# Kernel tuning notes

Hardware: AMD Instinct MI355X
Metric: run time of the kernel (lower is better)

Reference implementation:

```python
import jax, jax.numpy as jnp
import numpy as np

HEAD_SIZE = 128
N_EMBD = 128
B, T = 16, 2048


def setup_inputs() -> dict:
    key = jax.random.key(0)
    ks = jax.random.split(key, 7)
    s = 1.0 / np.sqrt(N_EMBD)
    return {
        "x": jax.random.normal(ks[0], (B, T, N_EMBD), dtype=jnp.float32),
        "Wq": jax.random.normal(ks[1], (N_EMBD, HEAD_SIZE), dtype=jnp.float32) * s,
        "bq": jax.random.normal(ks[2], (HEAD_SIZE,), dtype=jnp.float32) * s,
        "Wk": jax.random.normal(ks[3], (N_EMBD, HEAD_SIZE), dtype=jnp.float32) * s,
        "bk": jax.random.normal(ks[4], (HEAD_SIZE,), dtype=jnp.float32) * s,
        "Wv": jax.random.normal(ks[5], (N_EMBD, HEAD_SIZE), dtype=jnp.float32) * s,
        "bv": jax.random.normal(ks[6], (HEAD_SIZE,), dtype=jnp.float32) * s,
    }


def reference(x, Wq, bq, Wk, bk, Wv, bv):
    # Q/K/V projections: [B,T,E] @ [E,H] -> [B,T,H]
    q = jnp.einsum("bte,eh->bth", x, Wq) + bq
    k = jnp.einsum("bte,eh->bth", x, Wk) + bk
    v = jnp.einsum("bte,eh->bth", x, Wv) + bv
    scale = 1.0 / (HEAD_SIZE ** 0.5)
    scores = jnp.einsum("bqh,bkh->bqk", q, k) * scale  # [B,T,T]
    t = x.shape[1]
    tril = jnp.tril(jnp.ones((t, t), dtype=scores.dtype))
    # Faithful to original: scores*tril - 1e12*(1-tril)
    scores = scores * tril - 1e12 * (1.0 - tril)
    attn = jax.nn.softmax(scores, axis=-1)
    out = jnp.einsum("bqk,bkh->bqh", attn, v)  # [B,T,H]
    return out
```

## Files before the change

kernel.cpp:

```cpp
#include <hip/hip_runtime.h>
#include <math.h>

#define Bn 16
#define Tn 2048
#define En 128
#define Hn 128

typedef _Float16 f16;
typedef _Float16 f16x8 __attribute__((ext_vector_type(8)));
typedef _Float16 f16x4 __attribute__((ext_vector_type(4)));
typedef float    f32x4 __attribute__((ext_vector_type(4)));

#define MFMA16(a, b, c) __builtin_amdgcn_mfma_f32_16x16x32_f16(a, b, c, 0, 0, 0)

__global__ __launch_bounds__(256) void prep_wt(
    const float* __restrict__ Wq, const float* __restrict__ Wk,
    const float* __restrict__ Wv, f16* __restrict__ Wt)
{
    __shared__ f16 lds[En][Hn + 8];
    const int t = threadIdx.x;
    const int p = blockIdx.x;
    const float* W = (p == 0) ? Wq : (p == 1) ? Wk : Wv;

    #pragma unroll
    for (int i = 0; i < 16; ++i) {
        int idx = t + i * 256;
        int k = idx >> 5, n4 = idx & 31;
        float4 v = ((const float4*)W)[idx];
        #pragma unroll
        for (int j = 0; j < 4; ++j)
            lds[n4 * 4 + j][k] = (f16)(&v.x)[j];
    }
    __syncthreads();
    #pragma unroll
    for (int i = 0; i < 8; ++i) {
        int idx = t + i * 256;
        int n = idx >> 4, c = idx & 15;
        *(f16x8*)(Wt + p * En * Hn + n * Hn + c * 8) = *(const f16x8*)&lds[n][c * 8];
    }
}

__global__ __launch_bounds__(256, 2) void qkv_proj(
    const float* __restrict__ x, const f16* __restrict__ Wt,
    const float* __restrict__ bq, const float* __restrict__ bk,
    const float* __restrict__ bv,
    f16* __restrict__ Qo, f16* __restrict__ Ko, f16* __restrict__ Vtp)
{
    __shared__ f16 xs[64][En + 8];
    __shared__ f16 wt[Hn][En + 8];

    const int t = threadIdx.x;
    const long row0 = (long)blockIdx.x * 64;

    {
        const float4* xg = (const float4*)(x + row0 * En);
        #pragma unroll
        for (int i = 0; i < 8; ++i) {
            int idx = t + i * 256;
            int r = idx >> 5, c4 = idx & 31;
            float4 v = xg[idx];
            f16x4 h = { (f16)v.x, (f16)v.y, (f16)v.z, (f16)v.w };
            *(f16x4*)&xs[r][c4 * 4] = h;
        }
    }
    {
        const f16x8* wg = (const f16x8*)Wt;
        #pragma unroll
        for (int i = 0; i < 8; ++i) {
            int idx = t + i * 256;
            *(f16x8*)&wt[idx >> 4][(idx & 15) * 8] = wg[idx];
        }
    }
    __syncthreads();

    const int w = t >> 6, lane = t & 63;
    const int ln = lane & 15, hi = lane >> 4;

    f16x8 xf[4];
    #pragma unroll
    for (int kss = 0; kss < 4; ++kss)
        xf[kss] = *(const f16x8*)&xs[w * 16 + ln][kss * 32 + hi * 8];

    const float* bias[3] = { bq, bk, bv };
    const int b  = (int)(row0 >> 11);
    const int t0 = (int)(row0 & 2047);

    #pragma unroll
    for (int p = 0; p < 3; ++p) {
        f32x4 acc[8];
        #pragma unroll
        for (int i = 0; i < 8; ++i) acc[i] = (f32x4){0.f, 0.f, 0.f, 0.f};

        #pragma unroll
        for (int kss = 0; kss < 4; ++kss) {
            #pragma unroll
            for (int nt = 0; nt < 8; ++nt) {
                f16x8 bf = *(const f16x8*)&wt[nt * 16 + ln][kss * 32 + hi * 8];
                acc[nt] = MFMA16(xf[kss], bf, acc[nt]);
            }
        }
        __syncthreads();

        if (p < 2) {
            const f16x8* wg = (const f16x8*)(Wt + (p + 1) * En * Hn);
            #pragma unroll
            for (int i = 0; i < 8; ++i) {
                int idx = t + i * 256;
                *(f16x8*)&wt[idx >> 4][(idx & 15) * 8] = wg[idx];
            }
            const float scl = (p == 0)
                ? 0.08838834764831845f * 1.4426950408889634f : 1.0f;
            #pragma unroll
            for (int nt = 0; nt < 8; ++nt) {
                int col = nt * 16 + ln;
                float bvv = bias[p][col];
                #pragma unroll
                for (int reg = 0; reg < 4; ++reg)
                    xs[w * 16 + hi * 4 + reg][col] =
                        (f16)((acc[nt][reg] + bvv) * scl);
            }
            __syncthreads();
            f16* dst = (p == 0) ? Qo : Ko;
            #pragma unroll
            for (int i = 0; i < 4; ++i) {
                int idx = t + i * 256;
                int r = idx >> 4, c = idx & 15;
                *(f16x8*)(dst + (row0 + r) * Hn + c * 8) = *(const f16x8*)&xs[r][c * 8];
            }
        } else {
            f16 (*vbuf)[72] = reinterpret_cast<f16(*)[72]>(&wt[0][0]);
            #pragma unroll
            for (int nt = 0; nt < 8; ++nt) {
                int col = nt * 16 + ln;
                float bvv = bias[2][col];
                f16x4 hv;
                #pragma unroll
                for (int reg = 0; reg < 4; ++reg)
                    hv[reg] = (f16)(acc[nt][reg] + bvv);
                *(f16x4*)&vbuf[col][w * 16 + hi * 4] = hv;
            }
            __syncthreads();
            #pragma unroll
            for (int i = 0; i < 4; ++i) {
                int idx = t + i * 256;
                int h = idx >> 3, c = idx & 7;
                *(f16x8*)(Vtp + ((long)b * Hn + h) * Tn + t0 + c * 8) =
                    *(const f16x8*)&vbuf[h][c * 8];
            }
        }
    }
}

__global__ __launch_bounds__(256, 2) void attn_fwd(
    const f16* __restrict__ Qf, const f16* __restrict__ Kf,
    const f16* __restrict__ Vt, float* __restrict__ Out)
{
    __shared__ f16 ksh[64][En + 8];
    __shared__ f16 vsh[Hn][64 + 8];
    __shared__ f16 psh[4][16][64 + 8];

    const int t = threadIdx.x;
    const int w = t >> 6, lane = t & 63;
    const int ln = lane & 15, hi = lane >> 4;

    const int n = blockIdx.x;
    const int s = n >> 8, r = n & 255;
    const int j = r >> 4, bb = r & 15;
    const int qi = s ? (31 - j) : j;
    const int q0 = qi * 64;
    const int nkt = qi + 1;
    const long qbase = ((long)bb * Tn + q0) * Hn;
    const long kbase = (long)bb * Tn * Hn;
    const long vbase = (long)bb * Hn * Tn;

    f16x8 qfr[4];
    #pragma unroll
    for (int kss = 0; kss < 4; ++kss)
        qfr[kss] = *(const f16x8*)(Qf + qbase + (long)(16 * w + ln) * Hn
                                   + kss * 32 + hi * 8);

    f32x4 oacc[8];
    #pragma unroll
    for (int i = 0; i < 8; ++i) oacc[i] = (f32x4){0.f, 0.f, 0.f, 0.f};
    float mrow[4], lpart[4];
    #pragma unroll
    for (int i = 0; i < 4; ++i) { mrow[i] = -INFINITY; lpart[i] = 0.f; }

    {
        const f16* Kg = Kf + kbase;
        const f16* Vg = Vt + vbase;
        #pragma unroll
        for (int i = 0; i < 4; ++i) {
            int idx = t + i * 256;
            *(f16x8*)&ksh[idx >> 4][(idx & 15) * 8] =
                *(const f16x8*)(Kg + (long)(idx >> 4) * Hn + (idx & 15) * 8);
            *(f16x8*)&vsh[idx >> 3][(idx & 7) * 8] =
                *(const f16x8*)(Vg + (long)(idx >> 3) * Tn + (idx & 7) * 8);
        }
    }
    __syncthreads();

    for (int kt = 0; kt < nkt; ++kt) {
        const int k0 = kt * 64;
        const bool pre = (kt + 1 < nkt);

        f16x8 kreg[4], vreg[4];
        if (pre) {
            const f16* Kg = Kf + kbase + (long)(k0 + 64) * Hn;
            const f16* Vg = Vt + vbase + (k0 + 64);
            #pragma unroll
            for (int i = 0; i < 4; ++i) {
                int idx = t + i * 256;
                kreg[i] = *(const f16x8*)(Kg + (long)(idx >> 4) * Hn + (idx & 15) * 8);
                vreg[i] = *(const f16x8*)(Vg + (long)(idx >> 3) * Tn + (idx & 7) * 8);
            }
        }

        f32x4 sacc[4];
        #pragma unroll
        for (int i = 0; i < 4; ++i) sacc[i] = (f32x4){0.f, 0.f, 0.f, 0.f};
        __builtin_amdgcn_s_setprio(1);
        #pragma unroll
        for (int kss = 0; kss < 4; ++kss) {
            #pragma unroll
            for (int nt = 0; nt < 4; ++nt) {
                f16x8 bf = *(const f16x8*)&ksh[nt * 16 + ln][kss * 32 + hi * 8];
                sacc[nt] = MFMA16(qfr[kss], bf, sacc[nt]);
            }
        }
        __builtin_amdgcn_s_setprio(0);

        const bool diag = (kt == nkt - 1);
        float sv[4][4];
        #pragma unroll
        for (int reg = 0; reg < 4; ++reg) {
            int gq = q0 + 16 * w + hi * 4 + reg;
            #pragma unroll
            for (int nt = 0; nt < 4; ++nt) {
                float v = sacc[nt][reg];
                if (diag) v = (k0 + nt * 16 + ln <= gq) ? v : -1e12f;
                sv[reg][nt] = v;
            }
        }

        float worst = -INFINITY;
        #pragma unroll
        for (int reg = 0; reg < 4; ++reg) {
            float pm = fmaxf(fmaxf(sv[reg][0], sv[reg][1]),
                             fmaxf(sv[reg][2], sv[reg][3]));
            worst = fmaxf(worst, pm - mrow[reg]);
        }
        if (__any(worst > 11.5415603f)) {
            #pragma unroll
            for (int reg = 0; reg < 4; ++reg) {
                float mx = fmaxf(fmaxf(sv[reg][0], sv[reg][1]),
                                 fmaxf(sv[reg][2], sv[reg][3]));
                mx = fmaxf(mx, __shfl_xor(mx, 1));
                mx = fmaxf(mx, __shfl_xor(mx, 2));
                mx = fmaxf(mx, __shfl_xor(mx, 4));
                mx = fmaxf(mx, __shfl_xor(mx, 8));
                float mnew = fmaxf(mrow[reg], mx);
                float f = exp2f(mrow[reg] - mnew);
                mrow[reg] = mnew;
                lpart[reg] *= f;
                #pragma unroll
                for (int nt2 = 0; nt2 < 8; ++nt2) oacc[nt2][reg] *= f;
            }
        }

        #pragma unroll
        for (int reg = 0; reg < 4; ++reg) {
            float p0 = exp2f(sv[reg][0] - mrow[reg]);
            float p1 = exp2f(sv[reg][1] - mrow[reg]);
            float p2 = exp2f(sv[reg][2] - mrow[reg]);
            float p3 = exp2f(sv[reg][3] - mrow[reg]);
            lpart[reg] += (p0 + p1) + (p2 + p3);
            int qr = hi * 4 + reg;
            psh[w][qr][ln]      = (f16)p0;
            psh[w][qr][ln + 16] = (f16)p1;
            psh[w][qr][ln + 32] = (f16)p2;
            psh[w][qr][ln + 48] = (f16)p3;
        }

        __builtin_amdgcn_s_setprio(1);
        #pragma unroll
        for (int kss = 0; kss < 2; ++kss) {
            f16x8 pa = *(const f16x8*)&psh[w][ln][kss * 32 + hi * 8];
            #pragma unroll
            for (int nt = 0; nt < 8; ++nt) {
                f16x8 vb = *(const f16x8*)&vsh[nt * 16 + ln][kss * 32 + hi * 8];
                oacc[nt] = MFMA16(pa, vb, oacc[nt]);
            }
        }
        __builtin_amdgcn_s_setprio(0);

        __syncthreads();
        if (pre) {
            #pragma unroll
            for (int i = 0; i < 4; ++i) {
                int idx = t + i * 256;
                *(f16x8*)&ksh[idx >> 4][(idx & 15) * 8] = kreg[i];
                *(f16x8*)&vsh[idx >> 3][(idx & 7) * 8] = vreg[i];
            }
            __syncthreads();
        }
    }

    #pragma unroll
    for (int reg = 0; reg < 4; ++reg) {
        float lr = lpart[reg];
        lr += __shfl_xor(lr, 1);
        lr += __shfl_xor(lr, 2);
        lr += __shfl_xor(lr, 4);
        lr += __shfl_xor(lr, 8);
        float inv = 1.0f / lr;
        long orow = qbase + (long)(16 * w + hi * 4 + reg) * Hn;
        #pragma unroll
        for (int nt = 0; nt < 8; ++nt)
            Out[orow + nt * 16 + ln] = oacc[nt][reg] * inv;
    }
}

extern "C" void kernel_launch(void* const* d_in, const int* in_sizes, int n_in,
                              void* d_out, int out_size, void* d_ws, size_t ws_size,
                              hipStream_t stream)
{
    const float* x  = (const float*)d_in[0];
    const float* Wq = (const float*)d_in[1];
    const float* bq = (const float*)d_in[2];
    const float* Wk = (const float*)d_in[3];
    const float* bk = (const float*)d_in[4];
    const float* Wv = (const float*)d_in[5];
    const float* bv = (const float*)d_in[6];

    const size_t NE = (size_t)Bn * Tn * Hn;
    f16* Qf = (f16*)d_ws;
    f16* Kf = Qf + NE;
    f16* Vt = Kf + NE;
    f16* Wt = Vt + NE;

    prep_wt<<<dim3(3), dim3(256), 0, stream>>>(Wq, Wk, Wv, Wt);
    qkv_proj<<<dim3((Bn * Tn) / 64), dim3(256), 0, stream>>>(
        x, Wt, bq, bk, bv, Qf, Kf, Vt);
    attn_fwd<<<dim3(512), dim3(256), 0, stream>>>(Qf, Kf, Vt, (float*)d_out);
}
```

Measured before the change: 145.3 us.

## Load K/V and weight MFMA fragments directly from global memory, dropping LDS staging

The attention kernel no longer stages K and V tiles in shared memory with register prefetch and block-wide barriers. Each wave now loads its K and V MFMA fragments straight from global memory (relying on L1/L2) and no longer synchronises across waves per tile. The projection kernel likewise reads x and weight fragments directly from global memory instead of through LDS. This removes LDS traffic and barriers, but each of the four waves re-fetches the same K/V data, and the explicit prefetch that overlapped loads with compute is gone.

```diff
diff --git a/kernel.cpp b/kernel.cpp
--- a/kernel.cpp
+++ b/kernel.cpp
@@ -46,40 +46,25 @@
     const float* __restrict__ bv,
     f16* __restrict__ Qo, f16* __restrict__ Ko, f16* __restrict__ Vtp)
 {
-    __shared__ f16 xs[64][En + 8];
-    __shared__ f16 wt[Hn][En + 8];
+    __shared__ f16 ot[2][64][En + 8];
 
     const int t = threadIdx.x;
-    const long row0 = (long)blockIdx.x * 64;
-
-    {
-        const float4* xg = (const float4*)(x + row0 * En);
-        #pragma unroll
-        for (int i = 0; i < 8; ++i) {
-            int idx = t + i * 256;
-            int r = idx >> 5, c4 = idx & 31;
-            float4 v = xg[idx];
-            f16x4 h = { (f16)v.x, (f16)v.y, (f16)v.z, (f16)v.w };
-            *(f16x4*)&xs[r][c4 * 4] = h;
-        }
-    }
-    {
-        const f16x8* wg = (const f16x8*)Wt;
-        #pragma unroll
-        for (int i = 0; i < 8; ++i) {
-            int idx = t + i * 256;
-            *(f16x8*)&wt[idx >> 4][(idx & 15) * 8] = wg[idx];
-        }
-    }
-    __syncthreads();
-
     const int w = t >> 6, lane = t & 63;
     const int ln = lane & 15, hi = lane >> 4;
+    const long row0 = (long)blockIdx.x * 64;
 
     f16x8 xf[4];
-    #pragma unroll
-    for (int kss = 0; kss < 4; ++kss)
-        xf[kss] = *(const f16x8*)&xs[w * 16 + ln][kss * 32 + hi * 8];
+    {
+        const float* xr = x + (row0 + w * 16 + ln) * En;
+        #pragma unroll
+        for (int kss = 0; kss < 4; ++kss) {
+            float4 a = *(const float4*)(xr + kss * 32 + hi * 8);
+            float4 b = *(const float4*)(xr + kss * 32 + hi * 8 + 4);
+            f16x8 h = { (f16)a.x, (f16)a.y, (f16)a.z, (f16)a.w,
+                        (f16)b.x, (f16)b.y, (f16)b.z, (f16)b.w };
+            xf[kss] = h;
+        }
+    }
 
     const float* bias[3] = { bq, bk, bv };
     const int b  = (int)(row0 >> 11);
@@ -93,21 +78,17 @@
 
         #pragma unroll
         for (int kss = 0; kss < 4; ++kss) {
-            #pragma unroll
-            for (int nt = 0; nt < 8; ++nt) {
-                f16x8 bf = *(const f16x8*)&wt[nt * 16 + ln][kss * 32 + hi * 8];
-                acc[nt] = MFMA16(xf[kss], bf, acc[nt]);
-            }
-        }
-        __syncthreads();
+            f16x8 wf[8];
+            #pragma unroll
+            for (int nt = 0; nt < 8; ++nt)
+                wf[nt] = *(const f16x8*)(Wt + ((long)(p * Hn + nt * 16 + ln)) * En
+                                         + kss * 32 + hi * 8);
+            #pragma unroll
+            for (int nt = 0; nt < 8; ++nt)
+                acc[nt] = MFMA16(xf[kss], wf[nt], acc[nt]);
+        }
 
         if (p < 2) {
-            const f16x8* wg = (const f16x8*)(Wt + (p + 1) * En * Hn);
-            #pragma unroll
-            for (int i = 0; i < 8; ++i) {
-                int idx = t + i * 256;
-                *(f16x8*)&wt[idx >> 4][(idx & 15) * 8] = wg[idx];
-            }
             const float scl = (p == 0)
                 ? 0.08838834764831845f * 1.4426950408889634f : 1.0f;
             #pragma unroll
@@ -116,7 +97,7 @@
                 float bvv = bias[p][col];
                 #pragma unroll
                 for (int reg = 0; reg < 4; ++reg)
-                    xs[w * 16 + hi * 4 + reg][col] =
+                    ot[p][w * 16 + hi * 4 + reg][col] =
                         (f16)((acc[nt][reg] + bvv) * scl);
             }
             __syncthreads();
@@ -125,10 +106,12 @@
             for (int i = 0; i < 4; ++i) {
                 int idx = t + i * 256;
                 int r = idx >> 4, c = idx & 15;
-                *(f16x8*)(dst + (row0 + r) * Hn + c * 8) = *(const f16x8*)&xs[r][c * 8];
+                *(f16x8*)(dst + (row0 + r) * Hn + c * 8) =
+                    *(const f16x8*)&ot[p][r][c * 8];
             }
         } else {
-            f16 (*vbuf)[72] = reinterpret_cast<f16(*)[72]>(&wt[0][0]);
+            f16 (*vbuf)[80] = reinterpret_cast<f16(*)[80]>(&ot[0][0][0]);
+            __syncthreads();
             #pragma unroll
             for (int nt = 0; nt < 8; ++nt) {
                 int col = nt * 16 + ln;
@@ -155,8 +138,6 @@
     const f16* __restrict__ Qf, const f16* __restrict__ Kf,
     const f16* __restrict__ Vt, float* __restrict__ Out)
 {
-    __shared__ f16 ksh[64][En + 8];
-    __shared__ f16 vsh[Hn][64 + 8];
     __shared__ f16 psh[4][16][64 + 8];
 
     const int t = threadIdx.x;
@@ -170,8 +151,8 @@
     const int q0 = qi * 64;
     const int nkt = qi + 1;
     const long qbase = ((long)bb * Tn + q0) * Hn;
-    const long kbase = (long)bb * Tn * Hn;
-    const long vbase = (long)bb * Hn * Tn;
+    const f16* __restrict__ Kg = Kf + (long)bb * Tn * Hn;
+    const f16* __restrict__ Vg = Vt + (long)bb * Hn * Tn;
 
     f16x8 qfr[4];
     #pragma unroll
@@ -186,49 +167,34 @@
     #pragma unroll
     for (int i = 0; i < 4; ++i) { mrow[i] = -INFINITY; lpart[i] = 0.f; }
 
-    {
-        const f16* Kg = Kf + kbase;
-        const f16* Vg = Vt + vbase;
-        #pragma unroll
-        for (int i = 0; i < 4; ++i) {
-            int idx = t + i * 256;
-            *(f16x8*)&ksh[idx >> 4][(idx & 15) * 8] =
-                *(const f16x8*)(Kg + (long)(idx >> 4) * Hn + (idx & 15) * 8);
-            *(f16x8*)&vsh[idx >> 3][(idx & 7) * 8] =
-                *(const f16x8*)(Vg + (long)(idx >> 3) * Tn + (idx & 7) * 8);
-        }
-    }
-    __syncthreads();
-
     for (int kt = 0; kt < nkt; ++kt) {
         const int k0 = kt * 64;
-        const bool pre = (kt + 1 < nkt);
-
-        f16x8 kreg[4], vreg[4];
-        if (pre) {
-            const f16* Kg = Kf + kbase + (long)(k0 + 64) * Hn;
-            const f16* Vg = Vt + vbase + (k0 + 64);
-            #pragma unroll
-            for (int i = 0; i < 4; ++i) {
-                int idx = t + i * 256;
-                kreg[i] = *(const f16x8*)(Kg + (long)(idx >> 4) * Hn + (idx & 15) * 8);
-                vreg[i] = *(const f16x8*)(Vg + (long)(idx >> 3) * Tn + (idx & 7) * 8);
-            }
-        }
-
+
+        f16x8 kfr[4][4];
+        #pragma unroll
+        for (int kss = 0; kss < 4; ++kss)
+            #pragma unroll
+            for (int nt = 0; nt < 4; ++nt)
+                kfr[kss][nt] = *(const f16x8*)(Kg + (long)(k0 + nt * 16 + ln) * Hn
+                                               + kss * 32 + hi * 8);
         f32x4 sacc[4];
         #pragma unroll
         for (int i = 0; i < 4; ++i) sacc[i] = (f32x4){0.f, 0.f, 0.f, 0.f};
         __builtin_amdgcn_s_setprio(1);
         #pragma unroll
-        for (int kss = 0; kss < 4; ++kss) {
-            #pragma unroll
-            for (int nt = 0; nt < 4; ++nt) {
-                f16x8 bf = *(const f16x8*)&ksh[nt * 16 + ln][kss * 32 + hi * 8];
-                sacc[nt] = MFMA16(qfr[kss], bf, sacc[nt]);
-            }
-        }
+        for (int kss = 0; kss < 4; ++kss)
+            #pragma unroll
+            for (int nt = 0; nt < 4; ++nt)
+                sacc[nt] = MFMA16(qfr[kss], kfr[kss][nt], sacc[nt]);
         __builtin_amdgcn_s_setprio(0);
+
+        f16x8 vfr[2][8];
+        #pragma unroll
+        for (int ks2 = 0; ks2 < 2; ++ks2)
+            #pragma unroll
+            for (int nt = 0; nt < 8; ++nt)
+                vfr[ks2][nt] = *(const f16x8*)(Vg + (long)(nt * 16 + ln) * Tn
+                                               + k0 + ks2 * 32 + hi * 8);
 
         const bool diag = (kt == nkt - 1);
         float sv[4][4];
@@ -284,26 +250,13 @@
 
         __builtin_amdgcn_s_setprio(1);
         #pragma unroll
-        for (int kss = 0; kss < 2; ++kss) {
-            f16x8 pa = *(const f16x8*)&psh[w][ln][kss * 32 + hi * 8];
-            #pragma unroll
-            for (int nt = 0; nt < 8; ++nt) {
-                f16x8 vb = *(const f16x8*)&vsh[nt * 16 + ln][kss * 32 + hi * 8];
-                oacc[nt] = MFMA16(pa, vb, oacc[nt]);
-            }
+        for (int ks2 = 0; ks2 < 2; ++ks2) {
+            f16x8 pa = *(const f16x8*)&psh[w][ln][ks2 * 32 + hi * 8];
+            #pragma unroll
+            for (int nt = 0; nt < 8; ++nt)
+                oacc[nt] = MFMA16(pa, vfr[ks2][nt], oacc[nt]);
         }
         __builtin_amdgcn_s_setprio(0);
-
-        __syncthreads();
-        if (pre) {
-            #pragma unroll
-            for (int i = 0; i < 4; ++i) {
-                int idx = t + i * 256;
-                *(f16x8*)&ksh[idx >> 4][(idx & 15) * 8] = kreg[i];
-                *(f16x8*)&vsh[idx >> 3][(idx & 7) * 8] = vreg[i];
-            }
-            __syncthreads();
-        }
     }
 
     #pragma unroll
```

Measured after the change: 226.2 us. 55.7% more time.
